# Kernel tuning notes

Hardware: AMD Instinct MI355X
Metric: run time of the kernel (lower is better)

## Reference

```python
import jax, jax.numpy as jnp
import numpy as np

B, T, E, H = 256, 256, 384, 64

def setup_inputs() -> dict:
    key = jax.random.key(0)
    ks = jax.random.split(key, 4)
    s = 1.0 / np.sqrt(E)
    return {
        "x":  jax.random.normal(ks[0], (B, T, E), dtype=jnp.float32),
        "Wq": jax.random.normal(ks[1], (E, H), dtype=jnp.float32) * s,
        "bq": jnp.zeros((H,), dtype=jnp.float32),
        "Wk": jax.random.normal(ks[2], (E, H), dtype=jnp.float32) * s,
        "bk": jnp.zeros((H,), dtype=jnp.float32),
        "Wv": jax.random.normal(ks[3], (E, H), dtype=jnp.float32) * s,
        "bv": jnp.zeros((H,), dtype=jnp.float32),
    }

def reference(x, Wq, bq, Wk, bk, Wv, bv):
    # QKV projections: [B,T,E] @ [E,H] -> [B,T,H]
    q = x @ Wq + bq
    k = x @ Wk + bk
    v = x @ Wv + bv
    # attention scores (NOTE: original has no 1/sqrt(d) scaling)
    wei = jnp.einsum('bth,bsh->bts', q, k)  # [B,T,T]
    causal = jnp.tril(jnp.ones((T, T), dtype=bool))
    wei = jnp.where(causal, wei, -jnp.inf)
    wei = jax.nn.softmax(wei, axis=-1)
    # dropout is identity in eval mode
    out = jnp.einsum('bts,bsh->bth', wei, v)  # [B,T,H]
    return out
```

## Files before the change

kernel.cpp:

```cpp
#include <hip/hip_runtime.h>
#include <math.h>

#define Bb 256
#define Tt 256
#define Ee 384
#define Hh 64

typedef __attribute__((ext_vector_type(8))) short bf16x8;
typedef __attribute__((ext_vector_type(4))) float f32x4;

__device__ inline short f2bf(float f) {
    unsigned u = __float_as_uint(f);
    u += 0x7FFFu + ((u >> 16) & 1);
    return (short)(u >> 16);
}
__device__ inline float bf2f(short s) {
    return __uint_as_float(((unsigned)(unsigned short)s) << 16);
}

#define MFMA16(a, b, c) __builtin_amdgcn_mfma_f32_16x16x32_bf16((a), (b), (c), 0, 0, 0)

#define WLO_OFF 147456

#define K_HI 0
#define K_LO 32768
#define VF   65536
#define QH   98304
#define QL   116736
#define PBASE 98304
#define SMEM_BYTES 135168

__global__ __launch_bounds__(256) void prep_w(
    const float* __restrict__ Wq, const float* __restrict__ Wk,
    const float* __restrict__ Wv, unsigned char* __restrict__ wsp)
{
    int u = blockIdx.x * 256 + threadIdx.x;
    if (u >= 9216) return;
    int frag = u >> 6;
    int lu   = u & 63;
    int ec   = frag / 12, tct = frag - ec * 12;
    int koct = lu >> 4, n = lu & 15;
    int col  = tct * 16 + n;
    const float* Wm = (col < 64) ? Wq : ((col < 128) ? Wk : Wv);
    int c = col & 63;
    bf16x8 hi8, lo8;
    #pragma unroll
    for (int j = 0; j < 8; ++j) {
        float v = Wm[(ec * 32 + koct * 8 + j) * 64 + c];
        short h = f2bf(v);
        hi8[j] = h;
        lo8[j] = f2bf(v - bf2f(h));
    }
    *reinterpret_cast<bf16x8*>(wsp + frag * 1024 + lu * 16) = hi8;
    *reinterpret_cast<bf16x8*>(wsp + WLO_OFF + frag * 1024 + lu * 16) = lo8;
}

__global__ __launch_bounds__(1024) void head_fused(
    const float* __restrict__ x,
    const float* __restrict__ bq, const float* __restrict__ bk,
    const float* __restrict__ bv,
    const unsigned char* __restrict__ wsp,
    float* __restrict__ out)
{
    __shared__ __align__(16) unsigned char smem[SMEM_BYTES];

    const int b    = blockIdx.x;
    const int tid  = threadIdx.x;
    const int w    = tid >> 6;
    const int lane = tid & 63;
    const int quad = lane >> 4;
    const int nl   = lane & 15;
    const int ri   = w >> 2;
    const int cj   = w & 3;

    f32x4 acc[4][3];
    #pragma unroll
    for (int i = 0; i < 4; ++i)
        #pragma unroll
        for (int j = 0; j < 3; ++j) acc[i][j] = (f32x4){0,0,0,0};

    const float4* x4 = reinterpret_cast<const float4*>(x + (size_t)b * Tt * Ee);

    const int At  = ((tid >> 6) << 4) + (tid & 15);
    const int Ako = (tid >> 4) & 3;
    const float4* xsrc = x4 + At * 96 + Ako * 2;

    float4 pa0 = xsrc[0], pa1 = xsrc[1];
    {
        float v[8] = {pa0.x, pa0.y, pa0.z, pa0.w, pa1.x, pa1.y, pa1.z, pa1.w};
        bf16x8 hi8, lo8;
        #pragma unroll
        for (int j = 0; j < 8; ++j) {
            short h = f2bf(v[j]);
            hi8[j] = h;
            lo8[j] = f2bf(v[j] - bf2f(h));
        }
        *reinterpret_cast<bf16x8*>(smem + tid * 16) = hi8;
        *reinterpret_cast<bf16x8*>(smem + 16384 + tid * 16) = lo8;
    }
    pa0 = xsrc[8]; pa1 = xsrc[9];

    for (int ec = 0; ec < 12; ++ec) {
        __syncthreads();
        const int bufr = (ec & 1) * 32768;
        bf16x8 bh[3], bl[3];
        #pragma unroll
        for (int ct = 0; ct < 3; ++ct) {
            size_t o = (size_t)(ec * 12 + cj * 3 + ct) * 1024 + lane * 16;
            bh[ct] = *reinterpret_cast<const bf16x8*>(wsp + o);
            bl[ct] = *reinterpret_cast<const bf16x8*>(wsp + WLO_OFF + o);
        }
        if (ec < 11) {
            float v[8] = {pa0.x, pa0.y, pa0.z, pa0.w, pa1.x, pa1.y, pa1.z, pa1.w};
            bf16x8 hi8, lo8;
            #pragma unroll
            for (int j = 0; j < 8; ++j) {
                short h = f2bf(v[j]);
                hi8[j] = h;
                lo8[j] = f2bf(v[j] - bf2f(h));
            }
            int nb = (1 - (ec & 1)) * 32768;
            *reinterpret_cast<bf16x8*>(smem + nb + tid * 16) = hi8;
            *reinterpret_cast<bf16x8*>(smem + nb + 16384 + tid * 16) = lo8;
        }
        if (ec < 10) { pa0 = xsrc[(ec + 2) * 8]; pa1 = xsrc[(ec + 2) * 8 + 1]; }

        #pragma unroll
        for (int rt = 0; rt < 4; ++rt) {
            int ao = bufr + (4 * ri + rt) * 1024 + lane * 16;
            bf16x8 ah = *reinterpret_cast<bf16x8*>(smem + ao);
            bf16x8 al = *reinterpret_cast<bf16x8*>(smem + ao + 16384);
            #pragma unroll
            for (int ct = 0; ct < 3; ++ct) {
                acc[rt][ct] = MFMA16(ah, bh[ct], acc[rt][ct]);
                acc[rt][ct] = MFMA16(al, bh[ct], acc[rt][ct]);
                acc[rt][ct] = MFMA16(ah, bl[ct], acc[rt][ct]);
            }
        }
    }
    __syncthreads();

    #pragma unroll
    for (int ct = 0; ct < 3; ++ct) {
        int col = (cj * 3 + ct) * 16 + nl;
        float bias = (col < 64) ? bq[col] : (col < 128 ? bk[col - 64] : bv[col - 128]);
        #pragma unroll
        for (int rt = 0; rt < 4; ++rt)
            #pragma unroll
            for (int r = 0; r < 4; ++r) acc[rt][ct][r] += bias;
    }

    #pragma unroll
    for (int ct = 0; ct < 3; ++ct) {
        int col = (cj * 3 + ct) * 16 + nl;
        #pragma unroll
        for (int rt = 0; rt < 4; ++rt) {
            #pragma unroll
            for (int r = 0; r < 4; ++r) {
                float val = acc[rt][ct][r];
                int s = ri * 64 + rt * 16 + quad * 4 + r;
                if (col >= 64 && col < 128) {
                    int h = col - 64;
                    int addr = ((s >> 4) * 2 + (h >> 5)) * 1024
                             + ((((h & 31) >> 3) * 16 + (s & 15)) * 8 + (h & 7)) * 2;
                    short hi = f2bf(val);
                    short lo = f2bf(val - bf2f(hi));
                    *reinterpret_cast<short*>(smem + K_HI + addr) = hi;
                    *reinterpret_cast<short*>(smem + K_LO + addr) = lo;
                } else if (col >= 128) {
                    int h = col - 128, sl = s & 31;
                    int addr = ((s >> 5) * 4 + (h >> 4)) * 1024
                             + (((sl >> 3) * 16 + (h & 15)) * 8 + (sl & 7)) * 2;
                    *reinterpret_cast<short*>(smem + VF + addr) = f2bf(val);
                }
            }
        }
    }

    auto writeQhalf = [&](int half) {
        #pragma unroll
        for (int ct = 0; ct < 3; ++ct) {
            int col = (cj * 3 + ct) * 16 + nl;
            if (col < 64) {
                #pragma unroll
                for (int rt = 0; rt < 4; ++rt) {
                    #pragma unroll
                    for (int r = 0; r < 4; ++r) {
                        float val = acc[rt][ct][r];
                        int s = ri * 64 + rt * 16 + quad * 4 + r;
                        int rloc = s & 127;
                        short hi = f2bf(val);
                        short lo = f2bf(val - bf2f(hi));
                        *reinterpret_cast<short*>(smem + QH + (rloc * 72 + col) * 2) = hi;
                        *reinterpret_cast<short*>(smem + QL + (rloc * 72 + col) * 2) = lo;
                    }
                }
            }
        }
    };
    bf16x8 qh0, qh1, ql0, ql1;
    auto readQ = [&]() {
        int rloc = (16 * w + nl) & 127;
        int base = rloc * 144;
        qh0 = *reinterpret_cast<bf16x8*>(smem + QH + base + quad * 16);
        qh1 = *reinterpret_cast<bf16x8*>(smem + QH + base + 64 + quad * 16);
        ql0 = *reinterpret_cast<bf16x8*>(smem + QL + base + quad * 16);
        ql1 = *reinterpret_cast<bf16x8*>(smem + QL + base + 64 + quad * 16);
    };

    if (ri < 2) writeQhalf(0);
    __syncthreads();
    if (w < 8) readQ();
    __syncthreads();
    if (ri >= 2) writeQhalf(1);
    __syncthreads();
    if (w >= 8) readQ();
    __syncthreads();

    f32x4 oacc[4];
    #pragma unroll
    for (int i = 0; i < 4; ++i) oacc[i] = (f32x4){0,0,0,0};
    float lsum = 0.f;
    const int t0 = w * 16;
    unsigned char* pb = smem + PBASE + w * 1344;
    const int npairs = (w >> 1) + 1;

    for (int p = 0; p < npairs; ++p) {
        #pragma unroll
        for (int hf = 0; hf < 2; ++hf) {
            int st = 2 * p + hf;
            f32x4 s0 = (f32x4){0,0,0,0}, s1 = (f32x4){0,0,0,0};
            int kb = st * 2048 + lane * 16;
            bf16x8 kh0 = *reinterpret_cast<bf16x8*>(smem + K_HI + kb);
            bf16x8 kh1 = *reinterpret_cast<bf16x8*>(smem + K_HI + kb + 1024);
            bf16x8 kl0 = *reinterpret_cast<bf16x8*>(smem + K_LO + kb);
            bf16x8 kl1 = *reinterpret_cast<bf16x8*>(smem + K_LO + kb + 1024);
            s0 = MFMA16(qh0, kh0, s0);
            s1 = MFMA16(qh1, kh1, s1);
            s0 = MFMA16(ql0, kh0, s0);
            s1 = MFMA16(ql1, kh1, s1);
            s0 = MFMA16(qh0, kl0, s0);
            s1 = MFMA16(qh1, kl1, s1);
            int sg = st * 16 + nl;
            #pragma unroll
            for (int r = 0; r < 4; ++r) {
                int tg = t0 + quad * 4 + r;
                float sv = s0[r] + s1[r];
                float pv = (sg <= tg) ? __expf(sv) : 0.f;
                *reinterpret_cast<short*>(pb + ((quad * 4 + r) * 40 + hf * 16 + nl) * 2) = f2bf(pv);
            }
        }
        asm volatile("s_waitcnt lgkmcnt(0)" ::: "memory");
        bf16x8 pa = *reinterpret_cast<bf16x8*>(pb + (nl * 40 + quad * 8) * 2);
        float ls = 0.f;
        #pragma unroll
        for (int j = 0; j < 8; ++j) ls += bf2f(pa[j]);
        ls += __shfl_xor(ls, 16);
        ls += __shfl_xor(ls, 32);
        lsum += ls;
        int vb = p * 4096 + lane * 16;
        #pragma unroll
        for (int nt = 0; nt < 4; ++nt) {
            bf16x8 vf = *reinterpret_cast<bf16x8*>(smem + VF + vb + nt * 1024);
            oacc[nt] = MFMA16(pa, vf, oacc[nt]);
        }
    }

    float* lb_ = reinterpret_cast<float*>(pb + 1280);
    if (lane < 16) lb_[lane] = lsum;
    asm volatile("s_waitcnt lgkmcnt(0)" ::: "memory");
    float* ob = out + (size_t)b * Tt * Hh + (size_t)t0 * Hh;
    #pragma unroll
    for (int r = 0; r < 4; ++r) {
        float inv = 1.0f / lb_[quad * 4 + r];
        #pragma unroll
        for (int nt = 0; nt < 4; ++nt)
            ob[(quad * 4 + r) * 64 + nt * 16 + nl] = oacc[nt][r] * inv;
    }
}

extern "C" void kernel_launch(void* const* d_in, const int* in_sizes, int n_in,
                              void* d_out, int out_size, void* d_ws, size_t ws_size,
                              hipStream_t stream) {
    const float* x  = (const float*)d_in[0];
    const float* Wq = (const float*)d_in[1];
    const float* bq = (const float*)d_in[2];
    const float* Wk = (const float*)d_in[3];
    const float* bk = (const float*)d_in[4];
    const float* Wv = (const float*)d_in[5];
    const float* bv = (const float*)d_in[6];
    float* out = (float*)d_out;
    unsigned char* wsp = (unsigned char*)d_ws;
    hipLaunchKernelGGL(prep_w, dim3(36), dim3(256), 0, stream, Wq, Wk, Wv, wsp);
    hipLaunchKernelGGL(head_fused, dim3(Bb), dim3(1024), 0, stream,
                       x, bq, bk, bv, wsp, out);
}
```

Baseline: 186.3 us.

## Stage projection weight fragments into LDS with async double-buffered global_load_lds

```diff
diff --git a/kernel.cpp b/kernel.cpp
--- a/kernel.cpp
+++ b/kernel.cpp
@@ -22,6 +22,7 @@
 
 #define WLO_OFF 147456
 
+#define BB0 65536
 #define K_HI 0
 #define K_LO 32768
 #define VF   65536
@@ -85,6 +86,23 @@
     const int Ako = (tid >> 4) & 3;
     const float4* xsrc = x4 + At * 96 + Ako * 2;
 
+    auto bgld = [&](int ecn) {
+        if (w < 12) {
+            int p = ecn & 1;
+            const unsigned char* ghi = wsp + (size_t)(ecn * 12 + w) * 1024 + (size_t)lane * 16;
+            const unsigned char* glo = ghi + WLO_OFF;
+            __builtin_amdgcn_global_load_lds(
+                (const __attribute__((address_space(1))) unsigned*)ghi,
+                (__attribute__((address_space(3))) unsigned*)(smem + BB0 + p * 24576 + w * 1024),
+                16, 0, 0);
+            __builtin_amdgcn_global_load_lds(
+                (const __attribute__((address_space(1))) unsigned*)glo,
+                (__attribute__((address_space(3))) unsigned*)(smem + BB0 + p * 24576 + 12288 + w * 1024),
+                16, 0, 0);
+        }
+    };
+
+    bgld(0);
     float4 pa0 = xsrc[0], pa1 = xsrc[1];
     {
         float v[8] = {pa0.x, pa0.y, pa0.z, pa0.w, pa1.x, pa1.y, pa1.z, pa1.w};
@@ -102,14 +120,7 @@
 
     for (int ec = 0; ec < 12; ++ec) {
         __syncthreads();
-        const int bufr = (ec & 1) * 32768;
-        bf16x8 bh[3], bl[3];
-        #pragma unroll
-        for (int ct = 0; ct < 3; ++ct) {
-            size_t o = (size_t)(ec * 12 + cj * 3 + ct) * 1024 + lane * 16;
-            bh[ct] = *reinterpret_cast<const bf16x8*>(wsp + o);
-            bl[ct] = *reinterpret_cast<const bf16x8*>(wsp + WLO_OFF + o);
-        }
+        if (ec < 11) bgld(ec + 1);
         if (ec < 11) {
             float v[8] = {pa0.x, pa0.y, pa0.z, pa0.w, pa1.x, pa1.y, pa1.z, pa1.w};
             bf16x8 hi8, lo8;
@@ -125,9 +136,18 @@
         }
         if (ec < 10) { pa0 = xsrc[(ec + 2) * 8]; pa1 = xsrc[(ec + 2) * 8 + 1]; }
 
+        const int ab = (ec & 1) * 32768;
+        const int bb = BB0 + (ec & 1) * 24576;
+        bf16x8 bh[3], bl[3];
+        #pragma unroll
+        for (int ct = 0; ct < 3; ++ct) {
+            int o = bb + (cj * 3 + ct) * 1024 + lane * 16;
+            bh[ct] = *reinterpret_cast<bf16x8*>(smem + o);
+            bl[ct] = *reinterpret_cast<bf16x8*>(smem + o + 12288);
+        }
         #pragma unroll
         for (int rt = 0; rt < 4; ++rt) {
-            int ao = bufr + (4 * ri + rt) * 1024 + lane * 16;
+            int ao = ab + (4 * ri + rt) * 1024 + lane * 16;
             bf16x8 ah = *reinterpret_cast<bf16x8*>(smem + ao);
             bf16x8 al = *reinterpret_cast<bf16x8*>(smem + ao + 16384);
             #pragma unroll
@@ -177,7 +197,7 @@
         }
     }
 
-    auto writeQhalf = [&](int half) {
+    auto writeQhalf = [&]() {
         #pragma unroll
         for (int ct = 0; ct < 3; ++ct) {
             int col = (cj * 3 + ct) * 16 + nl;
@@ -208,11 +228,11 @@
         ql1 = *reinterpret_cast<bf16x8*>(smem + QL + base + 64 + quad * 16);
     };
 
-    if (ri < 2) writeQhalf(0);
+    if (ri < 2) writeQhalf();
     __syncthreads();
     if (w < 8) readQ();
     __syncthreads();
-    if (ri >= 2) writeQhalf(1);
+    if (ri >= 2) writeQhalf();
     __syncthreads();
     if (w >= 8) readQ();
     __syncthreads();
```

Measured after the change: 182.8 us. About the same (-1.8%).

## Split fused head kernel into separate QKV GEMM and attention kernels

Applied to the files above, without the earlier changes.

```diff
diff --git a/kernel.cpp b/kernel.cpp
--- a/kernel.cpp
+++ b/kernel.cpp
@@ -20,15 +20,13 @@
 
 #define MFMA16(a, b, c) __builtin_amdgcn_mfma_f32_16x16x32_bf16((a), (b), (c), 0, 0, 0)
 
-#define WLO_OFF 147456
-
-#define K_HI 0
-#define K_LO 32768
-#define VF   65536
-#define QH   98304
-#define QL   116736
-#define PBASE 98304
-#define SMEM_BYTES 135168
+#define W_HI_OFF 0
+#define W_LO_OFF 147456
+#define QHI_OFF  294912
+#define QLO_OFF  (QHI_OFF + 8388608)
+#define KHI_OFF  (QLO_OFF + 8388608)
+#define KLO_OFF  (KHI_OFF + 8388608)
+#define VT_OFF   (KLO_OFF + 8388608)
 
 __global__ __launch_bounds__(256) void prep_w(
     const float* __restrict__ Wq, const float* __restrict__ Wk,
@@ -51,25 +49,24 @@
         hi8[j] = h;
         lo8[j] = f2bf(v - bf2f(h));
     }
-    *reinterpret_cast<bf16x8*>(wsp + frag * 1024 + lu * 16) = hi8;
-    *reinterpret_cast<bf16x8*>(wsp + WLO_OFF + frag * 1024 + lu * 16) = lo8;
-}
-
-__global__ __launch_bounds__(1024) void head_fused(
+    *reinterpret_cast<bf16x8*>(wsp + W_HI_OFF + frag * 1024 + lu * 16) = hi8;
+    *reinterpret_cast<bf16x8*>(wsp + W_LO_OFF + frag * 1024 + lu * 16) = lo8;
+}
+
+__global__ __launch_bounds__(512) void qkv_gemm(
     const float* __restrict__ x,
     const float* __restrict__ bq, const float* __restrict__ bk,
     const float* __restrict__ bv,
-    const unsigned char* __restrict__ wsp,
-    float* __restrict__ out)
+    unsigned char* __restrict__ wsp)
 {
-    __shared__ __align__(16) unsigned char smem[SMEM_BYTES];
-
-    const int b    = blockIdx.x;
+    __shared__ __align__(16) unsigned char smem[49664];
+
+    const int blk  = blockIdx.x;
+    const int b    = blk >> 1, half = blk & 1;
     const int tid  = threadIdx.x;
     const int w    = tid >> 6;
     const int lane = tid & 63;
-    const int quad = lane >> 4;
-    const int nl   = lane & 15;
+    const int quad = lane >> 4, nl = lane & 15;
     const int ri   = w >> 2;
     const int cj   = w & 3;
 
@@ -79,38 +76,16 @@
         #pragma unroll
         for (int j = 0; j < 3; ++j) acc[i][j] = (f32x4){0,0,0,0};
 
-    const float4* x4 = reinterpret_cast<const float4*>(x + (size_t)b * Tt * Ee);
-
+    const float4* x4 = reinterpret_cast<const float4*>(x) + (size_t)b * (Tt * Ee / 4);
     const int At  = ((tid >> 6) << 4) + (tid & 15);
     const int Ako = (tid >> 4) & 3;
-    const float4* xsrc = x4 + At * 96 + Ako * 2;
+    const float4* xsrc = x4 + (size_t)(half * 128 + At) * 96 + Ako * 2;
 
     float4 pa0 = xsrc[0], pa1 = xsrc[1];
-    {
-        float v[8] = {pa0.x, pa0.y, pa0.z, pa0.w, pa1.x, pa1.y, pa1.z, pa1.w};
-        bf16x8 hi8, lo8;
-        #pragma unroll
-        for (int j = 0; j < 8; ++j) {
-            short h = f2bf(v[j]);
-            hi8[j] = h;
-            lo8[j] = f2bf(v[j] - bf2f(h));
-        }
-        *reinterpret_cast<bf16x8*>(smem + tid * 16) = hi8;
-        *reinterpret_cast<bf16x8*>(smem + 16384 + tid * 16) = lo8;
-    }
-    pa0 = xsrc[8]; pa1 = xsrc[9];
 
     for (int ec = 0; ec < 12; ++ec) {
         __syncthreads();
-        const int bufr = (ec & 1) * 32768;
-        bf16x8 bh[3], bl[3];
-        #pragma unroll
-        for (int ct = 0; ct < 3; ++ct) {
-            size_t o = (size_t)(ec * 12 + cj * 3 + ct) * 1024 + lane * 16;
-            bh[ct] = *reinterpret_cast<const bf16x8*>(wsp + o);
-            bl[ct] = *reinterpret_cast<const bf16x8*>(wsp + WLO_OFF + o);
-        }
-        if (ec < 11) {
+        {
             float v[8] = {pa0.x, pa0.y, pa0.z, pa0.w, pa1.x, pa1.y, pa1.z, pa1.w};
             bf16x8 hi8, lo8;
             #pragma unroll
@@ -119,17 +94,24 @@
                 hi8[j] = h;
                 lo8[j] = f2bf(v[j] - bf2f(h));
             }
-            int nb = (1 - (ec & 1)) * 32768;
-            *reinterpret_cast<bf16x8*>(smem + nb + tid * 16) = hi8;
-            *reinterpret_cast<bf16x8*>(smem + nb + 16384 + tid * 16) = lo8;
-        }
-        if (ec < 10) { pa0 = xsrc[(ec + 2) * 8]; pa1 = xsrc[(ec + 2) * 8 + 1]; }
-
+            *reinterpret_cast<bf16x8*>(smem + tid * 16) = hi8;
+            *reinterpret_cast<bf16x8*>(smem + 8192 + tid * 16) = lo8;
+        }
+        __syncthreads();
+        if (ec < 11) { pa0 = xsrc[(ec + 1) * 8]; pa1 = xsrc[(ec + 1) * 8 + 1]; }
+
+        bf16x8 bh[3], bl[3];
+        #pragma unroll
+        for (int ct = 0; ct < 3; ++ct) {
+            size_t o = (size_t)(ec * 12 + cj * 3 + ct) * 1024 + lane * 16;
+            bh[ct] = *reinterpret_cast<const bf16x8*>(wsp + W_HI_OFF + o);
+            bl[ct] = *reinterpret_cast<const bf16x8*>(wsp + W_LO_OFF + o);
+        }
         #pragma unroll
         for (int rt = 0; rt < 4; ++rt) {
-            int ao = bufr + (4 * ri + rt) * 1024 + lane * 16;
+            int ao = (4 * ri + rt) * 1024 + lane * 16;
             bf16x8 ah = *reinterpret_cast<bf16x8*>(smem + ao);
-            bf16x8 al = *reinterpret_cast<bf16x8*>(smem + ao + 16384);
+            bf16x8 al = *reinterpret_cast<bf16x8*>(smem + ao + 8192);
             #pragma unroll
             for (int ct = 0; ct < 3; ++ct) {
                 acc[rt][ct] = MFMA16(ah, bh[ct], acc[rt][ct]);
@@ -153,75 +135,120 @@
     #pragma unroll
     for (int ct = 0; ct < 3; ++ct) {
         int col = (cj * 3 + ct) * 16 + nl;
-        #pragma unroll
-        for (int rt = 0; rt < 4; ++rt) {
+        if (col < 64) {
+            #pragma unroll
+            for (int rt = 0; rt < 4; ++rt)
+                #pragma unroll
+                for (int r = 0; r < 4; ++r) {
+                    float val = acc[rt][ct][r];
+                    int s = ri * 64 + rt * 16 + quad * 4 + r;
+                    short hi = f2bf(val);
+                    short lo = f2bf(val - bf2f(hi));
+                    *reinterpret_cast<short*>(smem + s * 128 + col * 2) = hi;
+                    *reinterpret_cast<short*>(smem + 16384 + s * 128 + col * 2) = lo;
+                }
+        }
+    }
+    __syncthreads();
+    #pragma unroll
+    for (int i = 0; i < 4; ++i) {
+        int u = tid + i * 512;
+        int sec = u >> 10, uu = u & 1023;
+        bf16x8 d = *reinterpret_cast<bf16x8*>(smem + u * 16);
+        size_t g = (sec ? QLO_OFF : QHI_OFF) + (size_t)b * 32768 + half * 16384 + (size_t)uu * 16;
+        *reinterpret_cast<bf16x8*>(wsp + g) = d;
+    }
+    __syncthreads();
+
+    #pragma unroll
+    for (int ct = 0; ct < 3; ++ct) {
+        int col = (cj * 3 + ct) * 16 + nl;
+        #pragma unroll
+        for (int rt = 0; rt < 4; ++rt)
             #pragma unroll
             for (int r = 0; r < 4; ++r) {
                 float val = acc[rt][ct][r];
                 int s = ri * 64 + rt * 16 + quad * 4 + r;
                 if (col >= 64 && col < 128) {
                     int h = col - 64;
-                    int addr = ((s >> 4) * 2 + (h >> 5)) * 1024
-                             + ((((h & 31) >> 3) * 16 + (s & 15)) * 8 + (h & 7)) * 2;
                     short hi = f2bf(val);
                     short lo = f2bf(val - bf2f(hi));
-                    *reinterpret_cast<short*>(smem + K_HI + addr) = hi;
-                    *reinterpret_cast<short*>(smem + K_LO + addr) = lo;
+                    *reinterpret_cast<short*>(smem + s * 128 + h * 2) = hi;
+                    *reinterpret_cast<short*>(smem + 16384 + s * 128 + h * 2) = lo;
                 } else if (col >= 128) {
-                    int h = col - 128, sl = s & 31;
-                    int addr = ((s >> 5) * 4 + (h >> 4)) * 1024
-                             + (((sl >> 3) * 16 + (h & 15)) * 8 + (sl & 7)) * 2;
-                    *reinterpret_cast<short*>(smem + VF + addr) = f2bf(val);
+                    int h = col - 128;
+                    *reinterpret_cast<short*>(smem + 32768 + h * 264 + s * 2) = f2bf(val);
                 }
             }
-        }
-    }
-
-    auto writeQhalf = [&](int half) {
-        #pragma unroll
-        for (int ct = 0; ct < 3; ++ct) {
-            int col = (cj * 3 + ct) * 16 + nl;
-            if (col < 64) {
-                #pragma unroll
-                for (int rt = 0; rt < 4; ++rt) {
-                    #pragma unroll
-                    for (int r = 0; r < 4; ++r) {
-                        float val = acc[rt][ct][r];
-                        int s = ri * 64 + rt * 16 + quad * 4 + r;
-                        int rloc = s & 127;
-                        short hi = f2bf(val);
-                        short lo = f2bf(val - bf2f(hi));
-                        *reinterpret_cast<short*>(smem + QH + (rloc * 72 + col) * 2) = hi;
-                        *reinterpret_cast<short*>(smem + QL + (rloc * 72 + col) * 2) = lo;
-                    }
-                }
-            }
-        }
-    };
-    bf16x8 qh0, qh1, ql0, ql1;
-    auto readQ = [&]() {
-        int rloc = (16 * w + nl) & 127;
-        int base = rloc * 144;
-        qh0 = *reinterpret_cast<bf16x8*>(smem + QH + base + quad * 16);
-        qh1 = *reinterpret_cast<bf16x8*>(smem + QH + base + 64 + quad * 16);
-        ql0 = *reinterpret_cast<bf16x8*>(smem + QL + base + quad * 16);
-        ql1 = *reinterpret_cast<bf16x8*>(smem + QL + base + 64 + quad * 16);
-    };
-
-    if (ri < 2) writeQhalf(0);
-    __syncthreads();
-    if (w < 8) readQ();
-    __syncthreads();
-    if (ri >= 2) writeQhalf(1);
-    __syncthreads();
-    if (w >= 8) readQ();
+    }
+    __syncthreads();
+    #pragma unroll
+    for (int i = 0; i < 6; ++i) {
+        int u = tid + i * 512;
+        bf16x8 d;
+        size_t g;
+        if (u < 2048) {
+            int sec = u >> 10, uu = u & 1023;
+            d = *reinterpret_cast<bf16x8*>(smem + u * 16);
+            g = (sec ? KLO_OFF : KHI_OFF) + (size_t)b * 32768 + half * 16384 + (size_t)uu * 16;
+        } else {
+            int uv = u - 2048, h = uv >> 4, oct = uv & 15;
+            d = *reinterpret_cast<bf16x8*>(smem + 32768 + h * 264 + oct * 16);
+            g = VT_OFF + (size_t)b * 32768 + (size_t)h * 512 + half * 256 + oct * 16;
+        }
+        *reinterpret_cast<bf16x8*>(wsp + g) = d;
+    }
+}
+
+#define K_HI 0
+#define K_LO 32768
+#define VF   65536
+#define PBASE 98304
+__global__ __launch_bounds__(1024) void attn(
+    const unsigned char* __restrict__ wsp, float* __restrict__ out)
+{
+    __shared__ __align__(16) unsigned char smem[119808];
+
+    const int b    = blockIdx.x;
+    const int tid  = threadIdx.x;
+    const int w    = tid >> 6;
+    const int lane = tid & 63;
+    const int quad = lane >> 4, nl = lane & 15;
+    const int t0   = w * 16;
+
+    const unsigned char* qhi_b = wsp + QHI_OFF + (size_t)b * 32768;
+    const unsigned char* qlo_b = wsp + QLO_OFF + (size_t)b * 32768;
+    const unsigned char* khi_b = wsp + KHI_OFF + (size_t)b * 32768;
+    const unsigned char* klo_b = wsp + KLO_OFF + (size_t)b * 32768;
+    const unsigned char* vt_b  = wsp + VT_OFF  + (size_t)b * 32768;
+
+    #pragma unroll
+    for (int i = 0; i < 4; ++i) {
+        int t = w + i * 16;
+        int st = t & 15, ks = (t >> 4) & 1, lo = t >> 5;
+        const unsigned char* src = (lo ? klo_b : khi_b)
+            + (size_t)(st * 16 + nl) * 128 + ks * 64 + quad * 16;
+        bf16x8 d = *reinterpret_cast<const bf16x8*>(src);
+        *reinterpret_cast<bf16x8*>(smem + (lo ? K_LO : K_HI) + (st * 2 + ks) * 1024 + lane * 16) = d;
+    }
+    #pragma unroll
+    for (int i = 0; i < 2; ++i) {
+        int t = w + i * 16;
+        int p = t >> 2, nt = t & 3;
+        const unsigned char* src = vt_b + (size_t)(nt * 16 + nl) * 512 + (p * 32 + quad * 8) * 2;
+        bf16x8 d = *reinterpret_cast<const bf16x8*>(src);
+        *reinterpret_cast<bf16x8*>(smem + VF + (p * 4 + nt) * 1024 + lane * 16) = d;
+    }
+    bf16x8 qh0 = *reinterpret_cast<const bf16x8*>(qhi_b + (size_t)(t0 + nl) * 128 + quad * 16);
+    bf16x8 qh1 = *reinterpret_cast<const bf16x8*>(qhi_b + (size_t)(t0 + nl) * 128 + 64 + quad * 16);
+    bf16x8 ql0 = *reinterpret_cast<const bf16x8*>(qlo_b + (size_t)(t0 + nl) * 128 + quad * 16);
+    bf16x8 ql1 = *reinterpret_cast<const bf16x8*>(qlo_b + (size_t)(t0 + nl) * 128 + 64 + quad * 16);
     __syncthreads();
 
     f32x4 oacc[4];
     #pragma unroll
     for (int i = 0; i < 4; ++i) oacc[i] = (f32x4){0,0,0,0};
     float lsum = 0.f;
-    const int t0 = w * 16;
     unsigned char* pb = smem + PBASE + w * 1344;
     const int npairs = (w >> 1) + 1;
 
@@ -291,7 +318,7 @@
     const float* bv = (const float*)d_in[6];
     float* out = (float*)d_out;
     unsigned char* wsp = (unsigned char*)d_ws;
-    hipLaunchKernelGGL(prep_w, dim3(36), dim3(256), 0, stream, Wq, Wk, Wv, wsp);
-    hipLaunchKernelGGL(head_fused, dim3(Bb), dim3(1024), 0, stream,
-                       x, bq, bk, bv, wsp, out);
-}
+    hipLaunchKernelGGL(prep_w,   dim3(36),  dim3(256),  0, stream, Wq, Wk, Wv, wsp);
+    hipLaunchKernelGGL(qkv_gemm, dim3(512), dim3(512),  0, stream, x, bq, bk, bv, wsp);
+    hipLaunchKernelGGL(attn,     dim3(Bb),  dim3(1024), 0, stream, wsp, out);
+}
```

Result: slower. 192.4 us (+3.3%).
